# Kernel optimization log

Measured on AMD Instinct MI355X. Metric: run time of the kernel, lower is better.

Reference implementation:

```python
import jax, jax.numpy as jnp
import numpy as np

STRIDE = 1
PADDING = 1
DILATION = 1


def _conv_one(xi, wi):
    # xi: [C_in, H, W], wi: [C_out, C_in, ks, ks]
    out = jax.lax.conv_general_dilated(
        xi[None],  # [1, C_in, H, W]
        wi,
        window_strides=(STRIDE, STRIDE),
        padding=[(PADDING, PADDING), (PADDING, PADDING)],
        rhs_dilation=(DILATION, DILATION),
        dimension_numbers=("NCHW", "OIHW", "NCHW"),
    )
    return out[0]  # [C_out, H', W']


def setup_inputs() -> dict:
    key = jax.random.key(0)
    k1, k2, k3 = jax.random.split(key, 3)
    B, C_in, C_out, H, W, ks = 32, 32, 32, 256, 256, 3
    x = jax.random.normal(k1, (B, C_in, H, W), dtype=jnp.float32)
    weight = jax.random.normal(k2, (B, C_out, C_in, ks, ks), dtype=jnp.float32)
    bias = jax.random.normal(k3, (B, C_out), dtype=jnp.float32)
    return {"x": x, "weight": weight, "bias": bias}


def reference(x, weight, bias):
    # Per-sample conv: sample i of x convolved with weight[i].
    out = jax.vmap(_conv_one)(x, weight)  # [B, C_out, H', W']
    out = out + bias[:, :, None, None]
    return out
```

## Files before the change

### kernel.cpp

```cpp
#include <hip/hip_runtime.h>


#define BB 32
#define CI 32
#define CO 32
#define HH 256
#define WW 256

typedef unsigned int uint;
using short8  = __attribute__((ext_vector_type(8))) short;
using float4v = __attribute__((ext_vector_type(4))) float;

__device__ inline unsigned short f2bf(float f) {
    union { float f; uint u; } c; c.f = f;
    uint r = c.u + 0x7fffu + ((c.u >> 16) & 1u);
    return (unsigned short)(r >> 16);
}

__global__ __launch_bounds__(256)
void transpose_kernel(const float* __restrict__ x,
                      unsigned short* __restrict__ xt) {
    __shared__ float tile[CI * 260];
    const int h = blockIdx.x;
    const int b = blockIdx.y;
    const int t = threadIdx.x;

    const float* xp = x + (size_t)b * CI * HH * WW + (size_t)h * WW;
    #pragma unroll
    for (int i = 0; i < 8; ++i) {
        int idx = t + 256 * i;
        int w4  = idx & 63;
        int ci  = idx >> 6;
        float4 v = *(const float4*)(xp + (size_t)ci * HH * WW + w4 * 4);
        *(float4*)(&tile[ci * 260 + w4 * 4]) = v;
    }
    __syncthreads();

    const int w = t;
    uint dw[16];
    #pragma unroll
    for (int j = 0; j < 16; ++j) {
        uint lo = f2bf(tile[(2 * j) * 260 + w]);
        uint hi = f2bf(tile[(2 * j + 1) * 260 + w]);
        dw[j] = lo | (hi << 16);
    }
    unsigned short* op = xt + (((size_t)(b * HH + h)) * WW + w) * CI;
    #pragma unroll
    for (int q = 0; q < 4; ++q) {
        uint4 v = make_uint4(dw[4*q+0], dw[4*q+1], dw[4*q+2], dw[4*q+3]);
        *(uint4*)(op + q * 8) = v;
    }
}

#define TH 8
#define TW 32
#define XR (TH + 2)
#define XC (TW + 2)

__global__ __launch_bounds__(256)
void conv_mfma_kernel(const unsigned short* __restrict__ xt,
                      const float* __restrict__ wgt,
                      const float* __restrict__ bias,
                      float* __restrict__ out) {
    __shared__ unsigned short xs[XR * XC * CI];
    __shared__ unsigned short ws[CO * 9 * CI];

    const int tw = blockIdx.x;
    const int th = blockIdx.y;
    const int b  = blockIdx.z;
    const int t  = threadIdx.x;
    const int h0 = th * TH, w0 = tw * TW;

    const float* wp = wgt + (size_t)(b * CO) * CI * 9;
    for (int i = t; i < CO * CI * 9; i += 256) {
        int co  = i / (CI * 9);
        int rem = i - co * (CI * 9);
        int ci  = rem / 9;
        int tp  = rem - ci * 9;
        ws[(co * 9 + tp) * CI + ci] = f2bf(wp[i]);
    }
    for (int i = t; i < XR * XC * 4; i += 256) {
        int q   = i & 3;
        int pix = i >> 2;
        int r   = pix / XC;
        int c   = pix - r * XC;
        int h   = h0 - 1 + r;
        int w   = w0 - 1 + c;
        uint4 v = make_uint4(0, 0, 0, 0);
        if (h >= 0 && h < HH && w >= 0 && w < WW) {
            v = *(const uint4*)(xt + (((size_t)(b * HH + h)) * WW + w) * CI + q * 8);
        }
        *(uint4*)(&xs[pix * CI + q * 8]) = v;
    }
    __syncthreads();

    const int wv  = t >> 6;
    const int l   = t & 63;
    const int lp  = l & 15;
    const int lq  = l >> 4;
    const int co0 = (wv & 1) * 16;
    const int gb  = (wv >> 1) * 8;

    short8 A[9];
    #pragma unroll
    for (int tp = 0; tp < 9; ++tp)
        A[tp] = *(const short8*)(&ws[((co0 + lp) * 9 + tp) * CI + lq * 8]);

    float4v acc[8];
    #pragma unroll
    for (int g = 0; g < 8; ++g) acc[g] = {0.f, 0.f, 0.f, 0.f};

    #pragma unroll
    for (int g = 0; g < 8; ++g) {
        const int gg = gb + g;
        const int r  = gg >> 1;
        const int c0 = (gg & 1) * 16;
        #pragma unroll
        for (int kh = 0; kh < 3; ++kh) {
            #pragma unroll
            for (int kw = 0; kw < 3; ++kw) {
                short8 Bf = *(const short8*)(
                    &xs[((r + kh) * XC + (c0 + lp + kw)) * CI + lq * 8]);
                acc[g] = __builtin_amdgcn_mfma_f32_16x16x32_bf16(
                    A[kh * 3 + kw], Bf, acc[g], 0, 0, 0);
            }
        }
    }

    float bv[4];
    #pragma unroll
    for (int v = 0; v < 4; ++v) bv[v] = bias[b * CO + co0 + lq * 4 + v];

    #pragma unroll
    for (int g = 0; g < 8; ++g) {
        const int gg = gb + g;
        const int r  = gg >> 1;
        const int c0 = (gg & 1) * 16;
        const int h  = h0 + r;
        const int wpix = w0 + c0 + lp;
        #pragma unroll
        for (int v = 0; v < 4; ++v) {
            const int co = co0 + lq * 4 + v;
            out[(((size_t)(b * CO + co)) * HH + h) * WW + wpix] = acc[g][v] + bv[v];
        }
    }
}

#define FHT 16
#define FXR (FHT + 2)
#define LROW 264

__global__ __launch_bounds__(256)
void conv3x3_fallback(const float* __restrict__ x,
                      const float* __restrict__ wgt,
                      const float* __restrict__ bias,
                      float* __restrict__ out) {
    __shared__ float xs[FXR * LROW];
    __shared__ float wsh[CI * 9];
    const int co = blockIdx.x;
    const int ht = blockIdx.y;
    const int b  = blockIdx.z;
    const int tid = threadIdx.x;
    const int h0 = ht * FHT;
    for (int i = tid; i < CI * 9; i += 256)
        wsh[i] = wgt[((size_t)(b * CO + co) * CI) * 9 + i];
    for (int i = tid; i < FXR * 8; i += 256) {
        int row = i >> 3; int c = i & 7;
        int col = (c < 4) ? c : (256 + c);
        xs[row * LROW + col] = 0.0f;
    }
    const int wg = tid & 63, rp = tid >> 6;
    const int w0 = wg * 4, r0 = rp * 4;
    float acc[4][4];
    #pragma unroll
    for (int d = 0; d < 4; ++d)
        #pragma unroll
        for (int j = 0; j < 4; ++j) acc[d][j] = 0.0f;
    const float* xb = x + (size_t)(b * CI) * HH * WW;
    for (int ci = 0; ci < CI; ++ci) {
        __syncthreads();
        const float* xsrc = xb + (size_t)ci * HH * WW;
        for (int i = tid; i < FXR * 64; i += 256) {
            int row = i >> 6; int cq = i & 63;
            int gh = h0 - 1 + row;
            float4 v = make_float4(0.f, 0.f, 0.f, 0.f);
            if (gh >= 0 && gh < HH)
                v = *(const float4*)(xsrc + (size_t)gh * WW + cq * 4);
            *(float4*)(&xs[row * LROW + 4 + cq * 4]) = v;
        }
        __syncthreads();
        float wk[9];
        #pragma unroll
        for (int k = 0; k < 9; ++k) wk[k] = wsh[ci * 9 + k];
        #pragma unroll
        for (int xr = 0; xr < 6; ++xr) {
            const float* rowp = &xs[(r0 + xr) * LROW + w0];
            float xv[12];
            #pragma unroll
            for (int q = 0; q < 3; ++q) {
                float4 v = *(const float4*)(rowp + 4 * q);
                xv[4*q+0] = v.x; xv[4*q+1] = v.y; xv[4*q+2] = v.z; xv[4*q+3] = v.w;
            }
            #pragma unroll
            for (int dr = 0; dr < 4; ++dr) {
                const int kh = xr - dr;
                if (kh < 0 || kh > 2) continue;
                #pragma unroll
                for (int kw = 0; kw < 3; ++kw) {
                    const float wvv = wk[kh * 3 + kw];
                    #pragma unroll
                    for (int j = 0; j < 4; ++j)
                        acc[dr][j] += xv[j + kw + 3] * wvv;
                }
            }
        }
    }
    const float bv = bias[b * CO + co];
    float* ob = out + ((size_t)(b * CO + co) * HH + (h0 + r0)) * WW + w0;
    #pragma unroll
    for (int dr = 0; dr < 4; ++dr) {
        float4 o;
        o.x = acc[dr][0] + bv; o.y = acc[dr][1] + bv;
        o.z = acc[dr][2] + bv; o.w = acc[dr][3] + bv;
        *(float4*)(ob + (size_t)dr * WW) = o;
    }
}

extern "C" void kernel_launch(void* const* d_in, const int* in_sizes, int n_in,
                              void* d_out, int out_size, void* d_ws, size_t ws_size,
                              hipStream_t stream) {
    const float* x    = (const float*)d_in[0];
    const float* wgt  = (const float*)d_in[1];
    const float* bias = (const float*)d_in[2];
    float* out        = (float*)d_out;

    const size_t need = (size_t)BB * HH * WW * CI * sizeof(unsigned short);
    if (ws_size >= need) {
        unsigned short* xt = (unsigned short*)d_ws;
        hipLaunchKernelGGL(transpose_kernel, dim3(HH, BB), dim3(256), 0, stream,
                           x, xt);
        hipLaunchKernelGGL(conv_mfma_kernel, dim3(WW / TW, HH / TH, BB), dim3(256),
                           0, stream, xt, wgt, bias, out);
    } else {
        hipLaunchKernelGGL(conv3x3_fallback, dim3(CO, HH / FHT, BB), dim3(256),
                           0, stream, x, wgt, bias, out);
    }
}
```

Baseline: 554.4 us.

## Precompute bf16 weights once, swizzle input LDS, share B fragments across both output-channel halves

Adds a separate kernel that converts the weights to bf16 in tap-major layout once per sample, so each conv block no longer redoes the conversion and the LDS weight staging. Each wave now loads A fragments for all 32 output channels straight from global into registers and reuses every input B fragment for two MFMAs. An XOR swizzle on the LDS input tile is meant to reduce bank conflicts. The cost is more VGPRs for A fragments and accumulators, which could lower occupancy, plus one extra small kernel launch.

```diff
diff --git a/kernel.cpp b/kernel.cpp
--- a/kernel.cpp
+++ b/kernel.cpp
@@ -52,18 +52,32 @@
     }
 }
 
+__global__ __launch_bounds__(256)
+void wconv_kernel(const float* __restrict__ wgt,
+                  unsigned short* __restrict__ wb) {
+    const int i = blockIdx.x * 256 + threadIdx.x;
+    const int bc  = i / 288;
+    const int rem = i - bc * 288;
+    const int ci  = rem / 9;
+    const int tap = rem - ci * 9;
+    wb[(bc * 9 + tap) * CI + ci] = f2bf(wgt[i]);
+}
+
 #define TH 8
 #define TW 32
 #define XR (TH + 2)
 #define XC (TW + 2)
 
+__device__ inline int swz_us(int pix, int q) {
+    return pix * CI + (((q ^ (pix >> 1)) & 3) << 3);
+}
+
 __global__ __launch_bounds__(256)
 void conv_mfma_kernel(const unsigned short* __restrict__ xt,
-                      const float* __restrict__ wgt,
+                      const unsigned short* __restrict__ wb,
                       const float* __restrict__ bias,
                       float* __restrict__ out) {
-    __shared__ unsigned short xs[XR * XC * CI];
-    __shared__ unsigned short ws[CO * 9 * CI];
+    __shared__ __align__(16) unsigned short xs[XR * XC * CI];
 
     const int tw = blockIdx.x;
     const int th = blockIdx.y;
@@ -71,14 +85,19 @@
     const int t  = threadIdx.x;
     const int h0 = th * TH, w0 = tw * TW;
 
-    const float* wp = wgt + (size_t)(b * CO) * CI * 9;
-    for (int i = t; i < CO * CI * 9; i += 256) {
-        int co  = i / (CI * 9);
-        int rem = i - co * (CI * 9);
-        int ci  = rem / 9;
-        int tp  = rem - ci * 9;
-        ws[(co * 9 + tp) * CI + ci] = f2bf(wp[i]);
-    }
+    const int wv  = t >> 6;
+    const int l   = t & 63;
+    const int lp  = l & 15;
+    const int lq  = l >> 4;
+
+    const unsigned short* wbb = wb + (size_t)(b * CO) * 9 * CI;
+    short8 A0[9], A1[9];
+    #pragma unroll
+    for (int tp = 0; tp < 9; ++tp) {
+        A0[tp] = *(const short8*)(wbb + ((lp)      * 9 + tp) * CI + lq * 8);
+        A1[tp] = *(const short8*)(wbb + ((16 + lp) * 9 + tp) * CI + lq * 8);
+    }
+
     for (int i = t; i < XR * XC * 4; i += 256) {
         int q   = i & 3;
         int pix = i >> 2;
@@ -90,58 +109,57 @@
         if (h >= 0 && h < HH && w >= 0 && w < WW) {
             v = *(const uint4*)(xt + (((size_t)(b * HH + h)) * WW + w) * CI + q * 8);
         }
-        *(uint4*)(&xs[pix * CI + q * 8]) = v;
+        *(uint4*)(&xs[swz_us(pix, q)]) = v;
     }
     __syncthreads();
 
-    const int wv  = t >> 6;
-    const int l   = t & 63;
-    const int lp  = l & 15;
-    const int lq  = l >> 4;
-    const int co0 = (wv & 1) * 16;
-    const int gb  = (wv >> 1) * 8;
-
-    short8 A[9];
-    #pragma unroll
-    for (int tp = 0; tp < 9; ++tp)
-        A[tp] = *(const short8*)(&ws[((co0 + lp) * 9 + tp) * CI + lq * 8]);
-
-    float4v acc[8];
-    #pragma unroll
-    for (int g = 0; g < 8; ++g) acc[g] = {0.f, 0.f, 0.f, 0.f};
-
-    #pragma unroll
-    for (int g = 0; g < 8; ++g) {
-        const int gg = gb + g;
+    float4v acc0[4], acc1[4];
+    #pragma unroll
+    for (int g = 0; g < 4; ++g) {
+        acc0[g] = {0.f, 0.f, 0.f, 0.f};
+        acc1[g] = {0.f, 0.f, 0.f, 0.f};
+    }
+
+    #pragma unroll
+    for (int g = 0; g < 4; ++g) {
+        const int gg = wv * 4 + g;
         const int r  = gg >> 1;
         const int c0 = (gg & 1) * 16;
         #pragma unroll
         for (int kh = 0; kh < 3; ++kh) {
             #pragma unroll
             for (int kw = 0; kw < 3; ++kw) {
-                short8 Bf = *(const short8*)(
-                    &xs[((r + kh) * XC + (c0 + lp + kw)) * CI + lq * 8]);
-                acc[g] = __builtin_amdgcn_mfma_f32_16x16x32_bf16(
-                    A[kh * 3 + kw], Bf, acc[g], 0, 0, 0);
+                const int p = (r + kh) * XC + (c0 + lp + kw);
+                short8 Bf = *(const short8*)(&xs[swz_us(p, lq)]);
+                acc0[g] = __builtin_amdgcn_mfma_f32_16x16x32_bf16(
+                    A0[kh * 3 + kw], Bf, acc0[g], 0, 0, 0);
+                acc1[g] = __builtin_amdgcn_mfma_f32_16x16x32_bf16(
+                    A1[kh * 3 + kw], Bf, acc1[g], 0, 0, 0);
             }
         }
     }
 
-    float bv[4];
-    #pragma unroll
-    for (int v = 0; v < 4; ++v) bv[v] = bias[b * CO + co0 + lq * 4 + v];
-
-    #pragma unroll
-    for (int g = 0; g < 8; ++g) {
-        const int gg = gb + g;
+    float bv0[4], bv1[4];
+    #pragma unroll
+    for (int v = 0; v < 4; ++v) {
+        bv0[v] = bias[b * CO + lq * 4 + v];
+        bv1[v] = bias[b * CO + 16 + lq * 4 + v];
+    }
+
+    #pragma unroll
+    for (int g = 0; g < 4; ++g) {
+        const int gg = wv * 4 + g;
         const int r  = gg >> 1;
         const int c0 = (gg & 1) * 16;
         const int h  = h0 + r;
         const int wpix = w0 + c0 + lp;
         #pragma unroll
         for (int v = 0; v < 4; ++v) {
-            const int co = co0 + lq * 4 + v;
-            out[(((size_t)(b * CO + co)) * HH + h) * WW + wpix] = acc[g][v] + bv[v];
+            const int co_l = lq * 4 + v;
+            out[(((size_t)(b * CO + co_l)) * HH + h) * WW + wpix] =
+                acc0[g][v] + bv0[v];
+            out[(((size_t)(b * CO + 16 + co_l)) * HH + h) * WW + wpix] =
+                acc1[g][v] + bv1[v];
         }
     }
 }
@@ -234,13 +252,18 @@
     const float* bias = (const float*)d_in[2];
     float* out        = (float*)d_out;
 
-    const size_t need = (size_t)BB * HH * WW * CI * sizeof(unsigned short);
+    const size_t xt_elems = (size_t)BB * HH * WW * CI;
+    const size_t wb_elems = (size_t)BB * CO * 9 * CI;
+    const size_t need = (xt_elems + wb_elems) * sizeof(unsigned short);
     if (ws_size >= need) {
-        unsigned short* xt = (unsigned short*)d_ws;
+        unsigned short* xtp = (unsigned short*)d_ws;
+        unsigned short* wbp = xtp + xt_elems;
         hipLaunchKernelGGL(transpose_kernel, dim3(HH, BB), dim3(256), 0, stream,
-                           x, xt);
+                           x, xtp);
+        hipLaunchKernelGGL(wconv_kernel, dim3((BB * CO * CI * 9) / 256), dim3(256),
+                           0, stream, wgt, wbp);
         hipLaunchKernelGGL(conv_mfma_kernel, dim3(WW / TW, HH / TH, BB), dim3(256),
-                           0, stream, xt, wgt, bias, out);
+                           0, stream, xtp, wbp, bias, out);
     } else {
         hipLaunchKernelGGL(conv3x3_fallback, dim3(CO, HH / FHT, BB), dim3(256),
                            0, stream, x, wgt, bias, out);
```

Measured after the change: 546.6 us. Within noise of the previous version (-1.4%).
